# Optimization experiments

Measured on AMD Instinct MI355X. Metric: run time of the kernel, lower is better.

Reference implementation:

```python
import jax, jax.numpy as jnp
import numpy as np

K = 1000      # subset size (hardcoded in SelectionHead: SubsetOperator(k=1000, hard=True))
TAU = 1.0     # gumbel-softmax temperature
EPS = float(np.finfo(np.float32).tiny)  # torch SubsetOperator uses np.finfo(np.float32).tiny


def setup_inputs() -> dict:
    key = jax.random.key(0)
    k1, k2 = jax.random.split(key)
    B, N = 4, 32768
    logits = jax.random.normal(k1, (B, N), dtype=jnp.float32)
    # gumbel noise sampled once (torch samples Gumbel(0,1) inside forward)
    gumbel = jax.random.gumbel(k2, (B, N), dtype=jnp.float32)
    return {"logits": logits, "gumbel": gumbel}


def _subset_operator(logits, gumbel):
    """Iterative Gumbel top-k relaxation (Xie & Ermon), hard straight-through."""
    scores0 = logits + gumbel                      # [B, N]
    zeros = jnp.zeros_like(scores0)

    @jax.checkpoint
    def body(carry, _):
        scores, onehot, khot = carry
        # mask out already-selected mass, renormalize via softmax
        scores = scores + jnp.log(jnp.maximum(1.0 - onehot, EPS))
        onehot = jax.nn.softmax(scores / TAU, axis=-1)
        return (scores, onehot, khot + onehot), None

    (_, _, khot), _ = jax.lax.scan(body, (scores0, zeros, zeros), None, length=K)

    # hard k-hot with straight-through estimator
    _, ind = jax.lax.top_k(khot, K)                # [B, K]
    b = khot.shape[0]
    khot_hard = zeros.at[jnp.arange(b)[:, None], ind].set(1.0)
    return khot_hard - jax.lax.stop_gradient(khot) + khot


def reference(logits, gumbel):
    values = jax.nn.sigmoid(jnp.max(logits, axis=1))          # [B]
    actions = _subset_operator(logits, gumbel)                # [B, N]
    logprobs = jax.nn.log_softmax(logits, axis=-1) * actions  # [B, N]
    return values, logprobs, actions
```

## Files before the change

kernel.cpp:

```cpp
#include <hip/hip_runtime.h>
#include <math.h>
#include <stdint.h>

#define NCOL 32768
#define NROW 4
#define KSEL 1000
#define TPB  1024
#define NW   16
#define SLC  32
#define U0   0xC0200000u
#define CAPW 448
#define QW   7


__device__ __forceinline__ float wred_sum_f(float v) {
#pragma unroll
  for (int m = 32; m; m >>= 1) v += __shfl_xor(v, m, 64);
  return v;
}
__device__ __forceinline__ float wred_max_f(float v) {
#pragma unroll
  for (int m = 32; m; m >>= 1) v = fmaxf(v, __shfl_xor(v, m, 64));
  return v;
}
__device__ __forceinline__ int wred_sum_i(int v) {
#pragma unroll
  for (int m = 32; m; m >>= 1) v += __shfl_xor(v, m, 64);
  return v;
}
__device__ __forceinline__ uint32_t fmap(float f) {
  int b = __float_as_int(f);
  return b >= 0 ? ((uint32_t)b ^ 0x80000000u) : ~(uint32_t)b;
}

__global__ __launch_bounds__(TPB) void selhead_kernel(
    const float* __restrict__ logits,
    const float* __restrict__ gumbel,
    float* __restrict__ out)
{
  const int row  = blockIdx.x >> 5;
  const int slc  = blockIdx.x & 31;
  const int tid  = threadIdx.x;
  const int lane = tid & 63;
  const int wv   = tid >> 6;
  const long rowoff = (long)row * NCOL;
  const float* lrow = logits + rowoff;
  const float* grow = gumbel + rowoff;
  const unsigned long long lmask_lt = (lane == 63) ? 0x7FFFFFFFFFFFFFFFull
                                                   : ((1ull << lane) - 1ull);

  __shared__ uint32_t lu[NW][CAPW];
  __shared__ uint32_t li[NW][CAPW];
  __shared__ float    redF[NW];
  __shared__ float    redM[NW];
  __shared__ int      redA[2][NW];
  __shared__ uint32_t redP[2][NW];
  __shared__ int      tlist[32];
  __shared__ int      tnum;
  __shared__ int      bc;

  if (tid == 0) tnum = 0;
  __syncthreads();

  float pse = 0.f, mxl = -INFINITY;
  uint32_t wbase = 0;
#pragma unroll
  for (int j = 0; j < 8; ++j) {
    const int c = tid + 1024 * j;
    const float4 lv = ((const float4*)lrow)[c];
    const float4 gv = ((const float4*)grow)[c];
    const float lq[4] = {lv.x, lv.y, lv.z, lv.w};
    const float gq[4] = {gv.x, gv.y, gv.z, gv.w};
#pragma unroll
    for (int q = 0; q < 4; ++q) {
      pse += __expf(lq[q]);
      mxl = fmaxf(mxl, lq[q]);
      const uint32_t u = fmap(lq[q] + gq[q]);
      const bool pred = (u >= U0);
      const unsigned long long mb = __ballot(pred);
      if (pred) {
        const uint32_t pos = wbase + (uint32_t)__popcll(mb & lmask_lt);
        if (pos < CAPW) { lu[wv][pos] = u; li[wv][pos] = (uint32_t)(4*c + q); }
      }
      wbase += (uint32_t)__popcll(mb);
    }
  }
  {
    float ws = wred_sum_f(pse);
    float wm = wred_max_f(mxl);
    if (lane == 0) { redF[wv] = ws; redM[wv] = wm; }
  }
  __syncthreads();
  float SE = 0.f, ML = -INFINITY;
#pragma unroll
  for (int i = 0; i < NW; ++i) { SE += redF[i]; ML = fmaxf(ML, redM[i]); }
  const float logZ = logf(SE);
  if (slc == 0 && tid == 0) out[row] = 1.0f / (1.0f + expf(-ML));

  const uint32_t nc = (wbase < CAPW) ? wbase : CAPW;
  uint32_t cu[QW], ci[QW];
#pragma unroll
  for (int s = 0; s < QW; ++s) {
    const uint32_t p = (uint32_t)(lane + s * 64);
    if (p < nc) { cu[s] = lu[wv][p]; ci[s] = li[wv][p]; }
    else        { cu[s] = 0u;        ci[s] = 0u;        }
  }

  uint32_t T = 0xC0000000u;
  int step = 0;
  for (int b = 22; b >= 0; b -= 2, ++step) {
    const uint32_t c01 = T | (1u << b);
    const uint32_t c10 = T | (2u << b);
    const uint32_t c11 = T | (3u << b);
    int n01 = 0; uint32_t pk = 0;
#pragma unroll
    for (int s = 0; s < QW; ++s) {
      n01 += (cu[s] >= c01) ? 1 : 0;
      pk  += ((cu[s] >= c10) ? 1u : 0u) + ((cu[s] >= c11) ? 0x10000u : 0u);
    }
    n01 = wred_sum_i(n01);
    pk  = (uint32_t)wred_sum_i((int)pk);
    if (lane == 0) { redA[step & 1][wv] = n01; redP[step & 1][wv] = pk; }
    __syncthreads();
    int t01 = 0; uint32_t tp = 0;
#pragma unroll
    for (int i = 0; i < NW; ++i) { t01 += redA[step & 1][i]; tp += redP[step & 1][i]; }
    const int t10 = (int)(tp & 0xFFFFu);
    const int t11 = (int)(tp >> 16);
    if      (t11 >= KSEL) T = c11;
    else if (t10 >= KSEL) T = c10;
    else if (t01 >= KSEL) T = c01;
  }

  int c_gt, M;
  {
    uint32_t pk2 = 0;
#pragma unroll
    for (int s = 0; s < QW; ++s)
      pk2 += ((cu[s] > T) ? 1u : 0u) + ((cu[s] == T) ? 0x10000u : 0u);
    pk2 = (uint32_t)wred_sum_i((int)pk2);
    if (lane == 0) redP[step & 1][wv] = pk2;
    __syncthreads();
    uint32_t tp = 0;
#pragma unroll
    for (int i = 0; i < NW; ++i) tp += redP[step & 1][i];
    c_gt = (int)(tp & 0xFFFFu);
    M    = (int)(tp >> 16);
  }
  const int rneed = KSEL - c_gt;

#pragma unroll
  for (int s = 0; s < QW; ++s)
    if (cu[s] == T) { int p = atomicAdd(&tnum, 1); if (p < 32) tlist[p] = (int)ci[s]; }
  __syncthreads();
  if (tid == 0) {
    int cut = 0x7FFFFFFF;
    if (M > rneed) {
      int mm = tnum; if (mm > 32) mm = 32;
      for (int i = 0; i < mm; ++i) {
        int c2 = 0;
        for (int j2 = 0; j2 < mm; ++j2) c2 += (tlist[j2] < tlist[i]) ? 1 : 0;
        if (c2 == rneed - 1) cut = tlist[i];
      }
    }
    bc = cut;
  }
  __syncthreads();
  const int idx_cut = bc;

  {
    const int col = slc * 1024 + tid;
    const float lf = lrow[col];
    const float gf = grow[col];
    const uint32_t u = fmap(lf + gf);
    const bool sel = (u > T) || ((u == T) && (col <= idx_cut));
    const float a = sel ? 1.0f : 0.0f;
    out[NROW + rowoff + col] = (lf - logZ) * a;
    out[NROW + (long)NROW * NCOL + rowoff + col] = a;
  }
}

extern "C" void kernel_launch(void* const* d_in, const int* in_sizes, int n_in,
                              void* d_out, int out_size, void* d_ws, size_t ws_size,
                              hipStream_t stream) {
  const float* logits = (const float*)d_in[0];
  const float* gumbel = (const float*)d_in[1];
  float* out = (float*)d_out;
  hipLaunchKernelGGL(selhead_kernel, dim3(NROW * SLC), dim3(TPB), 0, stream,
                     logits, gumbel, out);
}
```

Before: 75.33 us.

## Replace per-wave ballot compaction with block-wide prefix-sum candidate buffer

Candidate filtering now records a per-thread bitmask of scores at or above a float threshold instead of issuing a ballot and popcount per element. A wave scan plus a cross-wave prefix gives each thread its write offset into one shared candidate array, filled in a second pass that reloads the inputs. The radix threshold search then starts from the positive-float bit pattern and covers one more bit pair over the block-wide buffer. This removes the per-element ballots and the per-wave capacity limits, at the cost of a second global read of the row and an extra barrier. The result is correct only if at least 1000 scores per row reach the threshold.

After: 76.10 us. About the same (+1.0%).

```diff
diff --git a/kernel.cpp b/kernel.cpp
--- a/kernel.cpp
+++ b/kernel.cpp
@@ -8,9 +8,9 @@
 #define TPB  1024
 #define NW   16
 #define SLC  32
-#define U0   0xC0200000u
-#define CAPW 448
-#define QW   7
+#define FTH  2.5f
+#define CAPB 6144
+#define QW   6
 
 
 __device__ __forceinline__ float wred_sum_f(float v) {
@@ -27,10 +27,6 @@
 #pragma unroll
   for (int m = 32; m; m >>= 1) v += __shfl_xor(v, m, 64);
   return v;
-}
-__device__ __forceinline__ uint32_t fmap(float f) {
-  int b = __float_as_int(f);
-  return b >= 0 ? ((uint32_t)b ^ 0x80000000u) : ~(uint32_t)b;
 }
 
 __global__ __launch_bounds__(TPB) void selhead_kernel(
@@ -46,13 +42,12 @@
   const long rowoff = (long)row * NCOL;
   const float* lrow = logits + rowoff;
   const float* grow = gumbel + rowoff;
-  const unsigned long long lmask_lt = (lane == 63) ? 0x7FFFFFFFFFFFFFFFull
-                                                   : ((1ull << lane) - 1ull);
-
-  __shared__ uint32_t lu[NW][CAPW];
-  __shared__ uint32_t li[NW][CAPW];
+
+  __shared__ uint32_t lu[CAPB];
+  __shared__ uint32_t li[CAPB];
   __shared__ float    redF[NW];
   __shared__ float    redM[NW];
+  __shared__ int      swtot[NW];
   __shared__ int      redA[2][NW];
   __shared__ uint32_t redP[2][NW];
   __shared__ int      tlist[32];
@@ -60,13 +55,12 @@
   __shared__ int      bc;
 
   if (tid == 0) tnum = 0;
-  __syncthreads();
 
   float pse = 0.f, mxl = -INFINITY;
-  uint32_t wbase = 0;
+  uint32_t cmask = 0u;
 #pragma unroll
   for (int j = 0; j < 8; ++j) {
-    const int c = tid + 1024 * j;
+    const int c = tid + TPB * j;
     const float4 lv = ((const float4*)lrow)[c];
     const float4 gv = ((const float4*)grow)[c];
     const float lq[4] = {lv.x, lv.y, lv.z, lv.w};
@@ -75,40 +69,69 @@
     for (int q = 0; q < 4; ++q) {
       pse += __expf(lq[q]);
       mxl = fmaxf(mxl, lq[q]);
-      const uint32_t u = fmap(lq[q] + gq[q]);
-      const bool pred = (u >= U0);
-      const unsigned long long mb = __ballot(pred);
-      if (pred) {
-        const uint32_t pos = wbase + (uint32_t)__popcll(mb & lmask_lt);
-        if (pos < CAPW) { lu[wv][pos] = u; li[wv][pos] = (uint32_t)(4*c + q); }
-      }
-      wbase += (uint32_t)__popcll(mb);
-    }
+      if (lq[q] + gq[q] >= FTH) cmask |= (1u << (4 * j + q));
+    }
+  }
+  const int cnt = __popc(cmask);
+  int isc = cnt;
+#pragma unroll
+  for (int d = 1; d < 64; d <<= 1) {
+    int nb = __shfl_up(isc, d, 64);
+    if (lane >= d) isc += nb;
   }
   {
     float ws = wred_sum_f(pse);
     float wm = wred_max_f(mxl);
     if (lane == 0) { redF[wv] = ws; redM[wv] = wm; }
-  }
-  __syncthreads();
+    if (lane == 63) swtot[wv] = isc;
+  }
+  __syncthreads();
+  int base_ = isc - cnt;
+  int m = 0;
   float SE = 0.f, ML = -INFINITY;
 #pragma unroll
-  for (int i = 0; i < NW; ++i) { SE += redF[i]; ML = fmaxf(ML, redM[i]); }
+  for (int i = 0; i < NW; ++i) {
+    if (i < wv) base_ += swtot[i];
+    m += swtot[i];
+    SE += redF[i];
+    ML = fmaxf(ML, redM[i]);
+  }
+  if (m > CAPB) m = CAPB;
   const float logZ = logf(SE);
   if (slc == 0 && tid == 0) out[row] = 1.0f / (1.0f + expf(-ML));
 
-  const uint32_t nc = (wbase < CAPW) ? wbase : CAPW;
+  int pos = base_;
+#pragma unroll
+  for (int j = 0; j < 8; ++j) {
+    const int c = tid + TPB * j;
+    const float4 lv = ((const float4*)lrow)[c];
+    const float4 gv = ((const float4*)grow)[c];
+    const float lq[4] = {lv.x, lv.y, lv.z, lv.w};
+    const float gq[4] = {gv.x, gv.y, gv.z, gv.w};
+#pragma unroll
+    for (int q = 0; q < 4; ++q) {
+      if ((cmask >> (4 * j + q)) & 1u) {
+        if (pos < CAPB) {
+          lu[pos] = __float_as_uint(lq[q] + gq[q]);
+          li[pos] = (uint32_t)(4 * c + q);
+        }
+        ++pos;
+      }
+    }
+  }
+  __syncthreads();
+
   uint32_t cu[QW], ci[QW];
 #pragma unroll
   for (int s = 0; s < QW; ++s) {
-    const uint32_t p = (uint32_t)(lane + s * 64);
-    if (p < nc) { cu[s] = lu[wv][p]; ci[s] = li[wv][p]; }
-    else        { cu[s] = 0u;        ci[s] = 0u;        }
-  }
-
-  uint32_t T = 0xC0000000u;
+    const int p = tid + TPB * s;
+    if (p < m) { cu[s] = lu[p]; ci[s] = li[p]; }
+    else       { cu[s] = 0u;    ci[s] = 0u;    }
+  }
+
+  uint32_t T = 0x40000000u;
   int step = 0;
-  for (int b = 22; b >= 0; b -= 2, ++step) {
+  for (int b = 24; b >= 0; b -= 2, ++step) {
     const uint32_t c01 = T | (1u << b);
     const uint32_t c10 = T | (2u << b);
     const uint32_t c11 = T | (3u << b);
@@ -172,8 +195,9 @@
     const int col = slc * 1024 + tid;
     const float lf = lrow[col];
     const float gf = grow[col];
-    const uint32_t u = fmap(lf + gf);
-    const bool sel = (u > T) || ((u == T) && (col <= idx_cut));
+    const float s0 = lf + gf;
+    const uint32_t u = __float_as_uint(s0);
+    const bool sel = (s0 >= FTH) && ((u > T) || ((u == T) && (col <= idx_cut)));
     const float a = sel ? 1.0f : 0.0f;
     out[NROW + rowoff + col] = (lf - logZ) * a;
     out[NROW + (long)NROW * NCOL + rowoff + col] = a;
```
